# Optimization experiments

Measured on AMD Instinct MI355X. Metric: run time of the kernel, lower is better.

Reference implementation:

```python
import jax, jax.numpy as jnp
import numpy as np
import math

D = 2048  # hidden_size
B, S = 4, 2048
EPS = 1e-5


def _ln(z, g, b):
    m = jnp.mean(z, axis=-1, keepdims=True)
    v = jnp.mean(jnp.square(z - m), axis=-1, keepdims=True)
    return (z - m) * jax.lax.rsqrt(v + EPS) * g + b


def _rotate_half(x):
    h = x.shape[-1] // 2
    return jnp.concatenate([-x[..., h:], x[..., :h]], axis=-1)


def _mas_normalize(logits):
    m = jnp.max(jnp.abs(logits), axis=-1, keepdims=True)
    return logits / (m + 1e-9)


def setup_inputs() -> dict:
    key = jax.random.key(0)
    ks = jax.random.split(key, 12)
    std = 0.02
    return {
        "x": jax.random.normal(ks[0], (B, S, D), dtype=jnp.float32),
        "position_ids": jnp.arange(S, dtype=jnp.int32),
        "ln1_g": jnp.ones((D,), jnp.float32),
        "ln1_b": jnp.zeros((D,), jnp.float32),
        # stacked params for [q, k, v, o]
        "mu_w": std * jax.random.normal(ks[1], (4, D, D), dtype=jnp.float32),
        "mu_b": jnp.zeros((4, D), jnp.float32),
        "proto_w": std * jax.random.normal(ks[2], (4, D, D), dtype=jnp.float32),
        "gate": jnp.zeros((4, D), jnp.float32),
        "pt_w": std * jax.random.normal(ks[3], (4, D, D), dtype=jnp.float32),
        "pln_g": jnp.ones((4, D), jnp.float32),
        "pln_b": jnp.zeros((4, D), jnp.float32),
        "incoming": std * jax.random.normal(ks[4], (4, D, D), dtype=jnp.float32),
    }


def reference(x, position_ids, ln1_g, ln1_b, mu_w, mu_b, proto_w, gate,
              pt_w, pln_g, pln_b, incoming):
    d = x.shape[-1]
    inv_sqrt_d = 1.0 / math.sqrt(d)

    # proto_state = proto_weight + LN(Linear(incoming))  per module [4, D, D]
    prc = jnp.einsum('nij,noj->nio', incoming, pt_w)
    proto_state = proto_w + _ln(prc, pln_g[:, None, :], pln_b[:, None, :])

    ln1_out = _ln(x, ln1_g, ln1_b)            # [B,S,D]
    ctx = jnp.mean(ln1_out, axis=1)           # [B,D]

    # qkv computation outputs: silu(ln1_out @ mu_w.T + mu_b) for n in {q,k,v}
    comp = jax.nn.silu(jnp.einsum('bsd,nod->nbso', ln1_out, mu_w[:3])
                       + mu_b[:3][:, None, None, :])            # [3,B,S,D]
    # routing from context vector
    match_ctx = jnp.einsum('bd,nod->nbo', ctx, proto_state[:3]) * inv_sqrt_d
    routing = match_ctx + gate[:3][:, None, :]                  # [3,B,D]
    gating = _mas_normalize(routing)
    masked = gating[:, :, None, :] * comp                       # [3,B,S,D]
    q, k, v = masked[0], masked[1], masked[2]

    # RoPE over full hidden dim (num_heads == 1)
    seq = position_ids.shape[0]
    inv_freq = 1.0 / (10000.0 ** (jnp.arange(0, d, 2, dtype=jnp.float32) / d))
    t = jnp.arange(seq, dtype=jnp.float32)
    freqs = t[:, None] * inv_freq[None, :]
    emb = jnp.concatenate([freqs, freqs], axis=-1)              # [S,D]
    cos = jnp.cos(emb)[position_ids]
    sin = jnp.sin(emb)[position_ids]
    q = q * cos + _rotate_half(q) * sin
    k = k * cos + _rotate_half(k) * sin

    # causal single-head attention, scale 1/sqrt(head_dim=D)
    scores = jnp.einsum('bqd,bkd->bqk', q, k) * inv_sqrt_d      # [B,S,S]
    causal = jnp.tril(jnp.ones((seq, seq), dtype=bool))
    scores = jnp.where(causal, scores, jnp.finfo(scores.dtype).min)
    probs = jax.nn.softmax(scores, axis=-1)
    attn_out = jnp.einsum('bqk,bkd->bqd', probs, v)             # [B,S,D]

    # output SPL + routing
    ctx_o = jnp.mean(attn_out, axis=1)
    c_o = jax.nn.silu(jnp.einsum('bsd,od->bso', attn_out, mu_w[3]) + mu_b[3])
    match_o = jnp.einsum('bd,od->bo', ctx_o, proto_state[3]) * inv_sqrt_d
    gating_o = _mas_normalize(match_o + gate[3])
    x_out = x + gating_o[:, None, :] * c_o
    return x_out
```

## Files before the change

kernel.cpp:

```cpp
#include <hip/hip_runtime.h>
#include <hip/hip_bf16.h>

#define Dh 2048
#define Bh 4
#define Sh 2048
#define NROW 8192
#define HALF 1024
#define INV_SQRT_D 0.022097086912079608f
#define LNEPS 1e-5f

typedef __hip_bfloat16 bf16;
typedef short short8 __attribute__((ext_vector_type(8)));
typedef float f32x4 __attribute__((ext_vector_type(4)));

__device__ inline float warp_sum(float x) {
#pragma unroll
  for (int o = 32; o > 0; o >>= 1) x += __shfl_down(x, o);
  return x;
}
__device__ inline float warp_max(float x) {
#pragma unroll
  for (int o = 32; o > 0; o >>= 1) x = fmaxf(x, __shfl_down(x, o));
  return x;
}
__device__ inline float block_sum(float x, float* sm4) {
  x = warp_sum(x);
  int w = threadIdx.x >> 6;
  if ((threadIdx.x & 63) == 0) sm4[w] = x;
  __syncthreads();
  float r = sm4[0] + sm4[1] + sm4[2] + sm4[3];
  __syncthreads();
  return r;
}
__device__ inline float block_max(float x, float* sm4) {
  x = warp_max(x);
  int w = threadIdx.x >> 6;
  if ((threadIdx.x & 63) == 0) sm4[w] = x;
  __syncthreads();
  float r = fmaxf(fmaxf(sm4[0], sm4[1]), fmaxf(sm4[2], sm4[3]));
  __syncthreads();
  return r;
}

__device__ inline void gload_lds16(const void* g, void* lds) {
  __builtin_amdgcn_global_load_lds(
      (const __attribute__((address_space(1))) unsigned int*)(unsigned long long)g,
      (__attribute__((address_space(3))) unsigned int*)(unsigned long long)lds,
      16, 0, 0);
}

template <int MODE>
__global__ __launch_bounds__(512) void pgemm(
    const bf16* __restrict__ Aall, const bf16* __restrict__ Ball,
    void* __restrict__ Call, int N, int K, int lda, int ldb,
    long sAz, long sBz, long sCz,
    const float* __restrict__ e0, const float* __restrict__ e1,
    const float* __restrict__ e2) {
  const int bm0 = blockIdx.x * 256;
  const int bn0 = blockIdx.y * 256;
  if (MODE == 2 && bn0 > bm0 + 255) return;
  const int z = blockIdx.z;
  const bf16* A = Aall + (long)z * sAz;
  const bf16* B = Ball + (long)z * sBz;

  __shared__ __align__(16) char smem[98304];
  const int tid = threadIdx.x;
  const int l = tid & 63, w = tid >> 6;
  const int wr = w >> 2, wc = w & 3;

  f32x4 acc[8][4] = {};

  const int nt = (MODE == 3) ? ((bm0 + 256) >> 5) : (K >> 5);

  const int sg = (((l & 3) ^ ((l >> 3) & 3)) << 3);

  auto stageA = [&](int tt, int half) {
    char* dst = smem + (tt % 3) * 16384 + (half << 13) + (w << 10);
    int row = (half << 7) + (w << 4) + (l >> 2);
    gload_lds16(A + (long)(bm0 + row) * lda + (tt << 5) + sg, dst);
  };
  auto stageB = [&](int tt, int half) {
    char* dst = smem + 49152 + (tt % 3) * 16384 + (half << 13) + (w << 10);
    int row = (half << 7) + (w << 4) + (l >> 2);
    gload_lds16(B + (long)(bn0 + row) * ldb + (tt << 5) + sg, dst);
  };

  stageA(0, 0); stageA(0, 1); stageB(0, 0); stageB(0, 1);
  if (nt > 1) { stageA(1, 0); stageA(1, 1); stageB(1, 0); stageB(1, 1); }
  if (nt > 1) asm volatile("s_waitcnt vmcnt(4)" ::: "memory");
  else        asm volatile("s_waitcnt vmcnt(0)" ::: "memory");
  __builtin_amdgcn_sched_barrier(0);
  asm volatile("s_barrier" ::: "memory");

  const int rslot = (((l >> 4) ^ ((l >> 1) & 3)) << 4);

#define MFMA4(FR)                                                             \
  acc[FR][0] = __builtin_amdgcn_mfma_f32_16x16x32_bf16(xa##FR, bfv0, acc[FR][0], 0, 0, 0); \
  acc[FR][1] = __builtin_amdgcn_mfma_f32_16x16x32_bf16(xa##FR, bfv1, acc[FR][1], 0, 0, 0); \
  acc[FR][2] = __builtin_amdgcn_mfma_f32_16x16x32_bf16(xa##FR, bfv2, acc[FR][2], 0, 0, 0); \
  acc[FR][3] = __builtin_amdgcn_mfma_f32_16x16x32_bf16(xa##FR, bfv3, acc[FR][3], 0, 0, 0);

  for (int t = 0; t < nt; ++t) {
    const char* Ab = smem + (t % 3) * 16384;
    const char* Bb = smem + 49152 + (t % 3) * 16384;
    const int abyte = (((wr << 7) + (l & 15)) << 6) + rslot;
    const int bbyte = (((wc << 6) + (l & 15)) << 6) + rslot;

    short8 bfv0 = *(const short8*)(Bb + bbyte + 0 * 1024);
    short8 bfv1 = *(const short8*)(Bb + bbyte + 1 * 1024);
    short8 bfv2 = *(const short8*)(Bb + bbyte + 2 * 1024);
    short8 bfv3 = *(const short8*)(Bb + bbyte + 3 * 1024);
    short8 xa0 = *(const short8*)(Ab + abyte + 0 * 1024);
    short8 xa1 = *(const short8*)(Ab + abyte + 1 * 1024);
    short8 xa2 = *(const short8*)(Ab + abyte + 2 * 1024);
    short8 xa3 = *(const short8*)(Ab + abyte + 3 * 1024);
    if (t + 2 < nt) { stageA(t + 2, 0); stageB(t + 2, 0); }
    asm volatile("s_barrier" ::: "memory");
    asm volatile("s_waitcnt lgkmcnt(0)" ::: "memory");
    __builtin_amdgcn_sched_barrier(0);
    __builtin_amdgcn_s_setprio(1);
    MFMA4(0) MFMA4(1) MFMA4(2) MFMA4(3)
    __builtin_amdgcn_s_setprio(0);
    asm volatile("s_barrier" ::: "memory");

    short8 xa4 = *(const short8*)(Ab + abyte + 4 * 1024);
    short8 xa5 = *(const short8*)(Ab + abyte + 5 * 1024);
    short8 xa6 = *(const short8*)(Ab + abyte + 6 * 1024);
    short8 xa7 = *(const short8*)(Ab + abyte + 7 * 1024);
    if (t + 2 < nt) { stageA(t + 2, 1); stageB(t + 2, 1); }
    asm volatile("s_barrier" ::: "memory");
    asm volatile("s_waitcnt lgkmcnt(0)" ::: "memory");
    __builtin_amdgcn_sched_barrier(0);
    __builtin_amdgcn_s_setprio(1);
    MFMA4(4) MFMA4(5) MFMA4(6) MFMA4(7)
    __builtin_amdgcn_s_setprio(0);
    if (t < nt - 1) {
      if (t + 2 < nt) asm volatile("s_waitcnt vmcnt(4)" ::: "memory");
      else            asm volatile("s_waitcnt vmcnt(0)" ::: "memory");
      __builtin_amdgcn_sched_barrier(0);
      asm volatile("s_barrier" ::: "memory");
    }
  }
#undef MFMA4

  const int lc = l & 15, lr4 = (l >> 4) << 2;
#pragma unroll
  for (int fr = 0; fr < 8; ++fr) {
    int gr0 = bm0 + (wr << 7) + fr * 16 + lr4;
#pragma unroll
    for (int fc = 0; fc < 4; ++fc) {
      int gc = bn0 + (wc << 6) + fc * 16 + lc;
#pragma unroll
      for (int qv = 0; qv < 4; ++qv) {
        int gr = gr0 + qv;
        float a = acc[fr][fc][qv];
        if (MODE == 0) {
          ((float*)Call + (long)z * sCz)[(long)gr * N + gc] = a;
        } else if (MODE == 1) {
          float val = a + e0[z * Dh + gc];
          float sil = val / (1.f + __expf(-val));
          int bb = gr >> 11;
          float g = e1[(z * Bh + bb) * Dh + gc];
          ((bf16*)Call + (long)z * sCz)[(long)gr * N + gc] =
              __float2bfloat16(sil * g);
        } else if (MODE == 2) {
          ((float*)Call + (long)z * sCz)[(long)gr * N + gc] = a * INV_SQRT_D;
        } else if (MODE == 3) {
          ((bf16*)Call + (long)z * sCz)[(long)gr * N + gc] = __float2bfloat16(a);
        } else {
          float val = a + e0[gc];
          float sil = val / (1.f + __expf(-val));
          int bb = gr >> 11;
          ((float*)Call)[(long)gr * N + gc] =
              e2[(long)gr * N + gc] + e1[bb * Dh + gc] * sil;
        }
      }
    }
  }
}

__global__ __launch_bounds__(256) void cvt3_kernel(
    const float* __restrict__ s0, const float* __restrict__ s1,
    const float* __restrict__ s2, bf16* __restrict__ o0, bf16* __restrict__ o1,
    bf16* __restrict__ o2, long n) {
  const float* in = (blockIdx.y == 0) ? s0 : (blockIdx.y == 1) ? s1 : s2;
  bf16* out = (blockIdx.y == 0) ? o0 : (blockIdx.y == 1) ? o1 : o2;
  long i = ((long)blockIdx.x * 256 + threadIdx.x) * 4;
  if (i >= n) return;
  float4 v = *(const float4*)(in + i);
  out[i + 0] = __float2bfloat16(v.x);
  out[i + 1] = __float2bfloat16(v.y);
  out[i + 2] = __float2bfloat16(v.z);
  out[i + 3] = __float2bfloat16(v.w);
}

__global__ __launch_bounds__(256) void transpose_kernel(const bf16* __restrict__ in,
                                                        bf16* __restrict__ out) {
  __shared__ bf16 t[64][65];
  int b = blockIdx.z;
  int s0 = blockIdx.x * 64, d0 = blockIdx.y * 64;
  const bf16* ib = in + (long)b * Sh * Dh;
  bf16* ob = out + (long)b * Sh * Dh;
  int tx = threadIdx.x & 63, ty = threadIdx.x >> 6;
#pragma unroll
  for (int r = ty; r < 64; r += 4) t[r][tx] = ib[(long)(s0 + r) * Dh + d0 + tx];
  __syncthreads();
#pragma unroll
  for (int r = ty; r < 64; r += 4) ob[(long)(d0 + r) * Sh + s0 + tx] = t[tx][r];
}

__global__ __launch_bounds__(256) void ln1_kernel(const float* __restrict__ x,
    const float* __restrict__ g, const float* __restrict__ b, bf16* __restrict__ out) {
  __shared__ float sm4[4];
  long r = blockIdx.x;
  const float* row = x + r * Dh;
  float v[8];
  float s = 0.f, s2 = 0.f;
#pragma unroll
  for (int c = 0; c < 8; ++c) {
    float t = row[threadIdx.x + c * 256];
    v[c] = t; s += t; s2 += t * t;
  }
  s = block_sum(s, sm4);
  s2 = block_sum(s2, sm4);
  float mean = s * (1.f / Dh);
  float rstd = rsqrtf(s2 * (1.f / Dh) - mean * mean + LNEPS);
#pragma unroll
  for (int c = 0; c < 8; ++c) {
    int o = threadIdx.x + c * 256;
    out[r * Dh + o] = __float2bfloat16((v[c] - mean) * rstd * g[o] + b[o]);
  }
}

__global__ __launch_bounds__(256) void meanrow_kernel(const bf16* __restrict__ in,
                                                      float* __restrict__ outbd) {
  int gid = blockIdx.x * 256 + threadIdx.x;
  int s0 = blockIdx.y * 128;
  long base = ((long)(gid >> 11) * Sh + s0) * Dh + (gid & 2047);
  float s = 0.f;
  for (int t = 0; t < 128; ++t) s += __bfloat162float(in[base + (long)t * Dh]);
  atomicAdd(&outbd[gid], s * (1.f / Sh));
}

__global__ __launch_bounds__(256) void route_kernel(
    const float* __restrict__ prc, const float* __restrict__ proto_w,
    const float* __restrict__ pln_g, const float* __restrict__ pln_b,
    const float* __restrict__ gate, const float* __restrict__ ctx,
    float* __restrict__ routing, float* __restrict__ ps3) {
  __shared__ float sm4[4];
  int i = blockIdx.x, n = blockIdx.y;
  long rb = ((long)n * Dh + i) * Dh;
  float v[8];
  float s = 0.f, s2 = 0.f;
#pragma unroll
  for (int c = 0; c < 8; ++c) {
    float t = prc[rb + threadIdx.x + c * 256];
    v[c] = t; s += t; s2 += t * t;
  }
  s = block_sum(s, sm4);
  s2 = block_sum(s2, sm4);
  float mean = s * (1.f / Dh);
  float rstd = rsqrtf(s2 * (1.f / Dh) - mean * mean + LNEPS);
  if (n == 3) {
#pragma unroll
    for (int c = 0; c < 8; ++c) {
      int o = threadIdx.x + c * 256;
      float ps = proto_w[rb + o] + (v[c] - mean) * rstd * pln_g[3 * Dh + o] + pln_b[3 * Dh + o];
      ps3[(long)i * Dh + o] = ps;
    }
  } else {
    float acc[4] = {0.f, 0.f, 0.f, 0.f};
#pragma unroll
    for (int c = 0; c < 8; ++c) {
      int o = threadIdx.x + c * 256;
      float ps = proto_w[rb + o] + (v[c] - mean) * rstd * pln_g[n * Dh + o] + pln_b[n * Dh + o];
#pragma unroll
      for (int b = 0; b < 4; ++b) acc[b] += ps * ctx[b * Dh + o];
    }
    for (int b = 0; b < 4; ++b) {
      float r = block_sum(acc[b], sm4);
      if (threadIdx.x == 0)
        routing[(n * 4 + b) * Dh + i] = r * INV_SQRT_D + gate[n * Dh + i];
    }
  }
}

__global__ __launch_bounds__(256) void route_o_kernel(
    const float* __restrict__ ps3, const float* __restrict__ ctxo,
    const float* __restrict__ gate, float* __restrict__ routing) {
  __shared__ float sm4[4];
  int i = blockIdx.x;
  float acc[4] = {0.f, 0.f, 0.f, 0.f};
#pragma unroll
  for (int c = 0; c < 8; ++c) {
    int o = threadIdx.x + c * 256;
    float p = ps3[(long)i * Dh + o];
#pragma unroll
    for (int b = 0; b < 4; ++b) acc[b] += p * ctxo[b * Dh + o];
  }
  for (int b = 0; b < 4; ++b) {
    float r = block_sum(acc[b], sm4);
    if (threadIdx.x == 0)
      routing[(12 + b) * Dh + i] = r * INV_SQRT_D + gate[3 * Dh + i];
  }
}

__global__ __launch_bounds__(256) void masnorm_kernel(const float* __restrict__ rin,
                                                      float* __restrict__ gout) {
  __shared__ float sm4[4];
  long r = blockIdx.x;
  float m = 0.f;
#pragma unroll
  for (int c = 0; c < 8; ++c)
    m = fmaxf(m, fabsf(rin[r * Dh + threadIdx.x + c * 256]));
  m = block_max(m, sm4);
  float inv = 1.f / (m + 1e-9f);
#pragma unroll
  for (int c = 0; c < 8; ++c) {
    int o = threadIdx.x + c * 256;
    gout[r * Dh + o] = rin[r * Dh + o] * inv;
  }
}

__global__ __launch_bounds__(256) void rope_table_kernel(float* __restrict__ cosT,
                                                         float* __restrict__ sinT) {
  int idx = blockIdx.x * 256 + threadIdx.x;
  int t = idx >> 10, f = idx & 1023;
  float inv_freq = expf(-(float)f * (9.210340371976184f / 1024.f));
  float ang = (float)t * inv_freq;
  cosT[idx] = cosf(ang);
  sinT[idx] = sinf(ang);
}

__global__ __launch_bounds__(256) void rope_kernel(bf16* __restrict__ q, bf16* __restrict__ k,
    const int* __restrict__ pos, const float* __restrict__ cosT,
    const float* __restrict__ sinT) {
  long r = blockIdx.x;
  int s = (int)(r & (Sh - 1));
  int p = pos[s];
#pragma unroll
  for (int c = 0; c < 4; ++c) {
    int t = threadIdx.x + c * 256;
    float cv = cosT[(long)p * HALF + t];
    float sv = sinT[(long)p * HALF + t];
    long i1 = r * Dh + t, i2 = i1 + HALF;
    float q1 = __bfloat162float(q[i1]), q2 = __bfloat162float(q[i2]);
    q[i1] = __float2bfloat16(q1 * cv - q2 * sv);
    q[i2] = __float2bfloat16(q2 * cv + q1 * sv);
    float k1 = __bfloat162float(k[i1]), k2 = __bfloat162float(k[i2]);
    k[i1] = __float2bfloat16(k1 * cv - k2 * sv);
    k[i2] = __float2bfloat16(k2 * cv + k1 * sv);
  }
}

__global__ __launch_bounds__(256) void softmax_kernel(const float* __restrict__ scores,
                                                      bf16* __restrict__ probs) {
  __shared__ float buf[Sh];
  __shared__ float sm4[4];
  long r = blockIdx.x;
  int qi = (int)(r & (Sh - 1));
  const float* row = scores + r * (long)Sh;
  bf16* prow = probs + r * (long)Sh;
  int n = qi + 1;
  float m = -3.0e38f;
  for (int o = threadIdx.x; o < n; o += 256) {
    float x = row[o]; buf[o] = x; m = fmaxf(m, x);
  }
  m = block_max(m, sm4);
  float s = 0.f;
  for (int o = threadIdx.x; o < n; o += 256) {
    float e = __expf(buf[o] - m); buf[o] = e; s += e;
  }
  s = block_sum(s, sm4);
  float inv = 1.f / s;
  for (int o = threadIdx.x; o < n; o += 256) prow[o] = __float2bfloat16(buf[o] * inv);
  for (int o = n + (int)threadIdx.x; o < Sh; o += 256) prow[o] = __float2bfloat16(0.f);
}

extern "C" void kernel_launch(void* const* d_in, const int* in_sizes, int n_in,
                              void* d_out, int out_size, void* d_ws, size_t ws_size,
                              hipStream_t stream) {
  const float* x       = (const float*)d_in[0];
  const int*   pos     = (const int*)d_in[1];
  const float* ln1_g   = (const float*)d_in[2];
  const float* ln1_b   = (const float*)d_in[3];
  const float* mu_w    = (const float*)d_in[4];
  const float* mu_b    = (const float*)d_in[5];
  const float* proto_w = (const float*)d_in[6];
  const float* gate    = (const float*)d_in[7];
  const float* pt_w    = (const float*)d_in[8];
  const float* pln_g   = (const float*)d_in[9];
  const float* pln_b   = (const float*)d_in[10];
  const float* incoming= (const float*)d_in[11];

  char* w = (char*)d_ws;
  const long BF = 33554432L;
  bf16*  ln1    = (bf16*)(w);
  bf16*  qb     = (bf16*)(w + BF);
  bf16*  kb     = (bf16*)(w + 2 * BF);
  bf16*  vb     = (bf16*)(w + 3 * BF);
  bf16*  attn   = (bf16*)(w + 4 * BF);
  bf16*  mu_wb  = (bf16*)(w + 5 * BF);
  bf16*  ptw_b  = (bf16*)(w + 6 * BF);
  bf16*  vT     = ptw_b;
  bf16*  inc_b  = (bf16*)(w + 7 * BF);
  bf16*  probs  = inc_b;
  float* ps3    = (float*)(w + 8 * BF);
  float* cosT   = (float*)(w + 8 * BF + 16777216L);
  float* sinT   = cosT + (long)Sh * HALF;
  float* ctx    = sinT + (long)Sh * HALF;
  float* ctxo   = ctx + Bh * Dh;
  float* routing= ctxo + Bh * Dh;
  float* gating = routing + 16 * Dh;
  float* scores = (float*)d_out;

  const long DD4 = 4L * Dh * Dh;

  hipMemsetAsync(ctx, 0, 2L * Bh * Dh * sizeof(float), stream);

  rope_table_kernel<<<(Sh * HALF) / 256, 256, 0, stream>>>(cosT, sinT);
  cvt3_kernel<<<dim3(DD4 / 1024, 3), 256, 0, stream>>>(
      mu_w, incoming, pt_w, mu_wb, inc_b, ptw_b, DD4);
  ln1_kernel<<<NROW, 256, 0, stream>>>(x, ln1_g, ln1_b, ln1);
  meanrow_kernel<<<dim3(32, 16), 256, 0, stream>>>(ln1, ctx);
  pgemm<0><<<dim3(8, 8, 4), 512, 0, stream>>>(
      inc_b, ptw_b, scores, Dh, Dh, Dh, Dh,
      (long)Dh * Dh, (long)Dh * Dh, (long)Dh * Dh, nullptr, nullptr, nullptr);
  route_kernel<<<dim3(Dh, 4), 256, 0, stream>>>(scores, proto_w, pln_g, pln_b,
                                                gate, ctx, routing, ps3);
  masnorm_kernel<<<12, 256, 0, stream>>>(routing, gating);
  pgemm<1><<<dim3(32, 8, 3), 512, 0, stream>>>(
      ln1, mu_wb, qb, Dh, Dh, Dh, Dh,
      0L, (long)Dh * Dh, (long)NROW * Dh, mu_b, gating, nullptr);
  rope_kernel<<<NROW, 256, 0, stream>>>(qb, kb, pos, cosT, sinT);
  pgemm<2><<<dim3(8, 8, 4), 512, 0, stream>>>(
      qb, kb, scores, Sh, Dh, Dh, Dh,
      (long)Sh * Dh, (long)Sh * Dh, (long)Sh * Sh, nullptr, nullptr, nullptr);
  softmax_kernel<<<Bh * Sh, 256, 0, stream>>>(scores, probs);
  transpose_kernel<<<dim3(32, 32, 4), 256, 0, stream>>>(vb, vT);
  pgemm<3><<<dim3(8, 8, 4), 512, 0, stream>>>(
      probs, vT, attn, Dh, Sh, Sh, Sh,
      (long)Sh * Sh, (long)Dh * Sh, (long)Sh * Dh, nullptr, nullptr, nullptr);
  meanrow_kernel<<<dim3(32, 16), 256, 0, stream>>>(attn, ctxo);
  route_o_kernel<<<Dh, 256, 0, stream>>>(ps3, ctxo, gate, routing);
  masnorm_kernel<<<4, 256, 0, stream>>>(routing + 12 * Dh, gating + 12 * Dh);
  pgemm<4><<<dim3(32, 8, 1), 512, 0, stream>>>(
      attn, mu_wb + 3L * Dh * Dh, d_out, Dh, Dh, Dh, Dh,
      0L, 0L, 0L, mu_b + 3 * Dh, gating + 12 * Dh, x);
}
```

Before: 721.3 us.

## Software-pipeline LDS fragment loads across K-tiles with ping-pong B registers

Restructures the GEMM main loop so that the A and B fragments for the next K-tile are read from LDS during the current tile's MFMA work. B fragments alternate between two register sets, and the loop is unrolled by two. Barriers per tile drop from four to two, and the vmcnt waits are adjusted to match. The aim is to hide LDS read latency and cut synchronisation stalls. The cost is higher VGPR pressure, and correctness depends on nt always being even.

```diff
diff --git a/kernel.cpp b/kernel.cpp
--- a/kernel.cpp
+++ b/kernel.cpp
@@ -85,6 +85,10 @@
     gload_lds16(B + (long)(bn0 + row) * ldb + (tt << 5) + sg, dst);
   };
 
+  const int rslot = (((l >> 4) ^ ((l >> 1) & 3)) << 4);
+  const int abyte = (((wr << 7) + (l & 15)) << 6) + rslot;
+  const int bbyte = (((wc << 6) + (l & 15)) << 6) + rslot;
+
   stageA(0, 0); stageA(0, 1); stageB(0, 0); stageB(0, 1);
   if (nt > 1) { stageA(1, 0); stageA(1, 1); stageB(1, 0); stageB(1, 1); }
   if (nt > 1) asm volatile("s_waitcnt vmcnt(4)" ::: "memory");
@@ -92,56 +96,86 @@
   __builtin_amdgcn_sched_barrier(0);
   asm volatile("s_barrier" ::: "memory");
 
-  const int rslot = (((l >> 4) ^ ((l >> 1) & 3)) << 4);
-
-#define MFMA4(FR)                                                             \
-  acc[FR][0] = __builtin_amdgcn_mfma_f32_16x16x32_bf16(xa##FR, bfv0, acc[FR][0], 0, 0, 0); \
-  acc[FR][1] = __builtin_amdgcn_mfma_f32_16x16x32_bf16(xa##FR, bfv1, acc[FR][1], 0, 0, 0); \
-  acc[FR][2] = __builtin_amdgcn_mfma_f32_16x16x32_bf16(xa##FR, bfv2, acc[FR][2], 0, 0, 0); \
-  acc[FR][3] = __builtin_amdgcn_mfma_f32_16x16x32_bf16(xa##FR, bfv3, acc[FR][3], 0, 0, 0);
-
-  for (int t = 0; t < nt; ++t) {
-    const char* Ab = smem + (t % 3) * 16384;
-    const char* Bb = smem + 49152 + (t % 3) * 16384;
-    const int abyte = (((wr << 7) + (l & 15)) << 6) + rslot;
-    const int bbyte = (((wc << 6) + (l & 15)) << 6) + rslot;
-
-    short8 bfv0 = *(const short8*)(Bb + bbyte + 0 * 1024);
-    short8 bfv1 = *(const short8*)(Bb + bbyte + 1 * 1024);
-    short8 bfv2 = *(const short8*)(Bb + bbyte + 2 * 1024);
-    short8 bfv3 = *(const short8*)(Bb + bbyte + 3 * 1024);
-    short8 xa0 = *(const short8*)(Ab + abyte + 0 * 1024);
-    short8 xa1 = *(const short8*)(Ab + abyte + 1 * 1024);
-    short8 xa2 = *(const short8*)(Ab + abyte + 2 * 1024);
-    short8 xa3 = *(const short8*)(Ab + abyte + 3 * 1024);
-    if (t + 2 < nt) { stageA(t + 2, 0); stageB(t + 2, 0); }
-    asm volatile("s_barrier" ::: "memory");
-    asm volatile("s_waitcnt lgkmcnt(0)" ::: "memory");
-    __builtin_amdgcn_sched_barrier(0);
-    __builtin_amdgcn_s_setprio(1);
-    MFMA4(0) MFMA4(1) MFMA4(2) MFMA4(3)
-    __builtin_amdgcn_s_setprio(0);
-    asm volatile("s_barrier" ::: "memory");
-
-    short8 xa4 = *(const short8*)(Ab + abyte + 4 * 1024);
-    short8 xa5 = *(const short8*)(Ab + abyte + 5 * 1024);
-    short8 xa6 = *(const short8*)(Ab + abyte + 6 * 1024);
-    short8 xa7 = *(const short8*)(Ab + abyte + 7 * 1024);
-    if (t + 2 < nt) { stageA(t + 2, 1); stageB(t + 2, 1); }
-    asm volatile("s_barrier" ::: "memory");
-    asm volatile("s_waitcnt lgkmcnt(0)" ::: "memory");
-    __builtin_amdgcn_sched_barrier(0);
-    __builtin_amdgcn_s_setprio(1);
-    MFMA4(4) MFMA4(5) MFMA4(6) MFMA4(7)
-    __builtin_amdgcn_s_setprio(0);
-    if (t < nt - 1) {
-      if (t + 2 < nt) asm volatile("s_waitcnt vmcnt(4)" ::: "memory");
-      else            asm volatile("s_waitcnt vmcnt(0)" ::: "memory");
-      __builtin_amdgcn_sched_barrier(0);
-      asm volatile("s_barrier" ::: "memory");
-    }
-  }
-#undef MFMA4
+  short8 a0, a1, a2, a3, a4, a5, a6, a7;
+  short8 be0, be1, be2, be3, bo0, bo1, bo2, bo3;
+
+  {
+    const char* Ab_ = smem;
+    const char* Bb_ = smem + 49152;
+    a0 = *(const short8*)(Ab_ + abyte + 0 * 1024);
+    a1 = *(const short8*)(Ab_ + abyte + 1 * 1024);
+    a2 = *(const short8*)(Ab_ + abyte + 2 * 1024);
+    a3 = *(const short8*)(Ab_ + abyte + 3 * 1024);
+    be0 = *(const short8*)(Bb_ + bbyte + 0 * 1024);
+    be1 = *(const short8*)(Bb_ + bbyte + 1 * 1024);
+    be2 = *(const short8*)(Bb_ + bbyte + 2 * 1024);
+    be3 = *(const short8*)(Bb_ + bbyte + 3 * 1024);
+  }
+  asm volatile("s_waitcnt lgkmcnt(0)" ::: "memory");
+  __builtin_amdgcn_sched_barrier(0);
+
+#define MROW(R, AF, B0, B1, B2, B3)                                           \
+  acc[R][0] = __builtin_amdgcn_mfma_f32_16x16x32_bf16(AF, B0, acc[R][0], 0, 0, 0); \
+  acc[R][1] = __builtin_amdgcn_mfma_f32_16x16x32_bf16(AF, B1, acc[R][1], 0, 0, 0); \
+  acc[R][2] = __builtin_amdgcn_mfma_f32_16x16x32_bf16(AF, B2, acc[R][2], 0, 0, 0); \
+  acc[R][3] = __builtin_amdgcn_mfma_f32_16x16x32_bf16(AF, B3, acc[R][3], 0, 0, 0);
+
+#define TILE(T, bc0, bc1, bc2, bc3, bn0_, bn1_, bn2_, bn3_)                   \
+  {                                                                           \
+    const int t_ = (T);                                                       \
+    const char* Ab_ = smem + (t_ % 3) * 16384;                                \
+              \
+    a4 = *(const short8*)(Ab_ + abyte + 4 * 1024);                            \
+    a5 = *(const short8*)(Ab_ + abyte + 5 * 1024);                            \
+    a6 = *(const short8*)(Ab_ + abyte + 6 * 1024);                            \
+    a7 = *(const short8*)(Ab_ + abyte + 7 * 1024);                            \
+    if (t_ + 2 < nt) { stageA(t_ + 2, 0); stageB(t_ + 2, 0); }                \
+    __builtin_amdgcn_sched_barrier(0);                                        \
+    __builtin_amdgcn_s_setprio(1);                                            \
+    MROW(0, a0, bc0, bc1, bc2, bc3)                                           \
+    MROW(1, a1, bc0, bc1, bc2, bc3)                                           \
+    MROW(2, a2, bc0, bc1, bc2, bc3)                                           \
+    MROW(3, a3, bc0, bc1, bc2, bc3)                                           \
+    __builtin_amdgcn_s_setprio(0);                                            \
+    __builtin_amdgcn_sched_barrier(0);                                        \
+    asm volatile("s_waitcnt lgkmcnt(0)" ::: "memory");                        \
+    if (t_ + 2 < nt) asm volatile("s_waitcnt vmcnt(2)" ::: "memory");         \
+    else             asm volatile("s_waitcnt vmcnt(0)" ::: "memory");         \
+    __builtin_amdgcn_sched_barrier(0);                                        \
+    asm volatile("s_barrier" ::: "memory");                                   \
+        \
+    if (t_ + 1 < nt) {                                                        \
+      const char* An_ = smem + ((t_ + 1) % 3) * 16384;                        \
+      const char* Bn_ = smem + 49152 + ((t_ + 1) % 3) * 16384;                \
+      a0 = *(const short8*)(An_ + abyte + 0 * 1024);                          \
+      a1 = *(const short8*)(An_ + abyte + 1 * 1024);                          \
+      a2 = *(const short8*)(An_ + abyte + 2 * 1024);                          \
+      a3 = *(const short8*)(An_ + abyte + 3 * 1024);                          \
+      bn0_ = *(const short8*)(Bn_ + bbyte + 0 * 1024);                        \
+      bn1_ = *(const short8*)(Bn_ + bbyte + 1 * 1024);                        \
+      bn2_ = *(const short8*)(Bn_ + bbyte + 2 * 1024);                        \
+      bn3_ = *(const short8*)(Bn_ + bbyte + 3 * 1024);                        \
+    }                                                                         \
+    if (t_ + 2 < nt) { stageA(t_ + 2, 1); stageB(t_ + 2, 1); }                \
+    __builtin_amdgcn_sched_barrier(0);                                        \
+    __builtin_amdgcn_s_setprio(1);                                            \
+    MROW(4, a4, bc0, bc1, bc2, bc3)                                           \
+    MROW(5, a5, bc0, bc1, bc2, bc3)                                           \
+    MROW(6, a6, bc0, bc1, bc2, bc3)                                           \
+    MROW(7, a7, bc0, bc1, bc2, bc3)                                           \
+    __builtin_amdgcn_s_setprio(0);                                            \
+    __builtin_amdgcn_sched_barrier(0);                                        \
+    asm volatile("s_waitcnt lgkmcnt(0)" ::: "memory");                        \
+    __builtin_amdgcn_sched_barrier(0);                                        \
+    asm volatile("s_barrier" ::: "memory");                                   \
+  }
+
+  for (int t = 0; t < nt; t += 2) {
+    TILE(t,     be0, be1, be2, be3, bo0, bo1, bo2, bo3);
+    TILE(t + 1, bo0, bo1, bo2, bo3, be0, be1, be2, be3);
+  }
+#undef TILE
+#undef MROW
 
   const int lc = l & 15, lr4 = (l >> 4) << 2;
 #pragma unroll
```

After: 722.6 us. Within noise of the previous version (+0.2%).
